# Optimization experiments

Hardware: AMD Instinct MI355X
Metric: run time of the kernel (lower is better)

The kernel has to match this reference:

```python
import jax, jax.numpy as jnp
import numpy as np

MAX_BOXES = 20
IOU_THRESHOLD = 0.1
SCORE_THRESHOLD = 0.3
NUM_CLASSES = 80
N_BOXES = 10647  # YOLOv3 @416: 3*(13^2 + 26^2 + 52^2)


def setup_inputs() -> dict:
    key = jax.random.key(0)
    k1, k2, k3 = jax.random.split(key, 3)
    # boxes in [y1, x1, y2, x2] format (what tf.image.non_max_suppression expects)
    mins = jax.random.uniform(k1, (N_BOXES, 2), minval=0.0, maxval=400.0)
    sizes = jax.random.uniform(k2, (N_BOXES, 2), minval=10.0, maxval=120.0)
    boxes = jnp.concatenate([mins, mins + sizes], axis=1)  # [N,4]
    box_scores = jax.random.uniform(k3, (N_BOXES, NUM_CLASSES))  # [N,C]
    return {"boxes": boxes, "box_scores": box_scores}


def _iou_one_vs_all(box, boxes):
    # box [4], boxes [N,4], format [y1,x1,y2,x2]
    tl = jnp.maximum(box[:2], boxes[:, :2])
    br = jnp.minimum(box[2:], boxes[:, 2:])
    inter = jnp.prod(jnp.clip(br - tl, 0.0), axis=1)
    area1 = jnp.prod(box[2:] - box[:2])
    areas = jnp.prod(boxes[:, 2:] - boxes[:, :2], axis=1)
    union = area1 + areas - inter
    return jnp.where(union > 0, inter / union, 0.0)


def _nms_single_class(boxes, scores):
    """Greedy NMS for one class. Returns padded ([MAX_BOXES] int32 indices, [MAX_BOXES] bool valid).
    Matches tf.image.non_max_suppression semantics (suppress when IoU > threshold),
    applied after the score_threshold mask (invalid scores set to -inf)."""
    n = scores.shape[0]
    s0 = jnp.where(scores >= SCORE_THRESHOLD, scores, -jnp.inf)

    def body(i, state):
        s, idxs, valid = state
        j = jnp.argmax(s)
        ok = s[j] > -jnp.inf
        iou = _iou_one_vs_all(boxes[j], boxes)  # [N]
        suppress = (iou > IOU_THRESHOLD) | (jnp.arange(n) == j)
        s = jnp.where(ok & suppress, -jnp.inf, s)
        idxs = idxs.at[i].set(jnp.where(ok, j, -1).astype(jnp.int32))
        valid = valid.at[i].set(ok)
        return (s, idxs, valid)

    init = (s0, jnp.full((MAX_BOXES,), -1, jnp.int32), jnp.zeros((MAX_BOXES,), bool))
    _, idxs, valid = jax.lax.fori_loop(0, MAX_BOXES, body, init)
    return idxs, valid


def reference(boxes, box_scores):
    # Per-class greedy NMS, vectorized over classes with vmap.
    idxs, valid = jax.vmap(_nms_single_class, in_axes=(None, 1))(boxes, box_scores)  # [C,MAX_BOXES]
    c = box_scores.shape[1]
    classes = jnp.broadcast_to(jnp.arange(c, dtype=jnp.int32)[:, None], (c, MAX_BOXES))
    classes = jnp.where(valid, classes, -1)
    batch_idx = jnp.where(valid, 0, -1).astype(jnp.int32)
    # Fixed-shape (padded) analogue of the variable-length concat in the original:
    # rows are [batch_index, class, box_index]; invalid slots are -1.
    nms_final = jnp.stack([batch_idx, classes, idxs], axis=-1).reshape(1, c * MAX_BOXES, 3)
    boxes_1 = boxes[None]                 # [1,N,4]
    box_scores_t_1 = box_scores.T[None]   # [1,C,N]
    return boxes_1, box_scores_t_1, nms_final
```

## Files before the change

### kernel.cpp

```cpp
#include <hip/hip_runtime.h>
#include <math.h>

#define N_BOXES 10647
#define NUM_CLASSES 80
#define MAX_BOXES 20
#define IOU_T 0.1f
#define SCORE_T 0.3f

#define WND_T 0.992f

#define NT 1024
#define NWAVES (NT / 64)
#define WCAP 128

#define TROWS 64
#define TBLOCKS 167
#define CPBLOCKS 6
#define K1_BLOCKS (TBLOCKS + CPBLOCKS)

#define WSLOTS 8
#define SLOT_N (TBLOCKS * WSLOTS)
#define SENTINEL (~0ull)

#define OUT_OFF_SCORES (N_BOXES * 4)
#define OUT_OFF_NMS (N_BOXES * 4 + NUM_CLASSES * N_BOXES)

#define FOR_K(OP) OP(0) OP(1) OP(2) OP(3) OP(4) OP(5) OP(6) OP(7) OP(8) OP(9) OP(10)

__device__ __forceinline__ bool iou_gt(float jy1, float jx1, float jy2,
                                       float jx2, float area_j, float4 b) {
    float ty = fmaxf(jy1, b.x);
    float tx = fmaxf(jx1, b.y);
    float by = fminf(jy2, b.z);
    float bx = fminf(jx2, b.w);
    float dy = fmaxf(__fsub_rn(by, ty), 0.0f);
    float dx = fmaxf(__fsub_rn(bx, tx), 0.0f);
    float inter = __fmul_rn(dy, dx);
    if (!(inter > 0.0f)) return false;
    float area_i = __fmul_rn(__fsub_rn(b.z, b.x), __fsub_rn(b.w, b.y));
    float uni = __fsub_rn(__fadd_rn(area_j, area_i), inter);
    float iou = (uni > 0.0f) ? __fdiv_rn(inter, uni) : 0.0f;
    return iou > IOU_T;
}

__global__ __launch_bounds__(NT) void transpose_slots_kernel(
    const float* __restrict__ boxes, const float* __restrict__ scores,
    float* __restrict__ out, unsigned long long* __restrict__ ws) {
    const int tid = threadIdx.x;
    const int b = blockIdx.x;

    if (b >= TBLOCKS) {
        for (int q = (b - TBLOCKS) * NT + tid; q < N_BOXES;
             q += CPBLOCKS * NT) {
            ((float4*)out)[q] = ((const float4*)boxes)[q];
        }
        return;
    }

    __shared__ float lds[TROWS * 81];
    const int r0 = b * TROWS;
    const int nr = min(TROWS, N_BOXES - r0);

    const int nq = nr * 20;
    for (int q = tid; q < nq; q += NT) {
        const int r = q / 20;
        const int c4 = (q - r * 20) * 4;
        float4 v = *(const float4*)(scores + (r0 + r) * NUM_CLASSES + c4);
        float* dst = &lds[r * 81 + c4];
        dst[0] = v.x;
        dst[1] = v.y;
        dst[2] = v.z;
        dst[3] = v.w;
    }
    __syncthreads();

    const int r = tid & (TROWS - 1);
    const int chi = tid >> 6;
    #pragma unroll
    for (int p = 0; p < 5; ++p) {
        const int c = p * 16 + chi;
        float v = 0.0f;
        if (r < nr) {
            v = lds[r * 81 + c];
            out[OUT_OFF_SCORES + c * N_BOXES + r0 + r] = v;
        }
        const bool cand = (r < nr) && (v >= WND_T);
        const unsigned long long mask = __ballot(cand);
        unsigned long long* slot = ws + ((size_t)c * TBLOCKS + b) * WSLOTS;
        const int cnt = __popcll(mask);
        if (cnt <= WSLOTS) {
            if (cand) {
                const int rank =
                    __popcll(mask & ((1ull << r) - 1ull));
                slot[rank] =
                    ((unsigned long long)__float_as_uint(v) << 32) |
                    (0xFFFFFFFFu - (unsigned)(r0 + r));
            }
            if (r >= cnt && r < WSLOTS) slot[r] = 0ull;
        } else {
            if (r == 0) slot[0] = SENTINEL;
            if (r >= 1 && r < WSLOTS) slot[r] = 0ull;
        }
    }
}

__global__ __launch_bounds__(NT) void nms_kernel(
    const float* __restrict__ boxes, float* __restrict__ out,
    const unsigned long long* __restrict__ ws) {
    const int tid = threadIdx.x;
    const int c = blockIdx.x;
    const int wave = tid >> 6;
    const int lane = tid & 63;
    const float4* boxes4 = (const float4*)boxes;
    const float* col = out + OUT_OFF_SCORES + c * N_BOXES;

    __shared__ unsigned long long s_k[WCAP];
    __shared__ float4 s_b4[WCAP];
    __shared__ unsigned long long s_ks[WCAP];
    __shared__ float4 s_bs[WCAP];
    __shared__ __align__(16) unsigned long long s_mask[WCAP][2];
    __shared__ unsigned long long s_rk[2][NWAVES];
    __shared__ int s_out[MAX_BOXES];
    __shared__ int s_cnt, s_nsel, s_ovf;

    if (tid < MAX_BOXES) s_out[tid] = -1;
    if (tid == 0) { s_cnt = 0; s_nsel = 0; s_ovf = 0; }
    __syncthreads();

    const unsigned long long* wsl = ws + (size_t)c * SLOT_N;
    for (int q = tid; q < SLOT_N; q += NT) {
        unsigned long long s = wsl[q];
        bool val = false;
        if (s != 0ull) {
            if ((unsigned)(s >> 32) >= 0x3F800000u) {
                s_ovf = 1;
            } else {
                val = true;
            }
        }
        const unsigned long long m = __ballot(val);
        int basew = 0;
        if (lane == 0 && m) basew = atomicAdd(&s_cnt, __popcll(m));
        basew = __shfl(basew, 0);
        if (val) {
            const int pos = basew + __popcll(m & ((1ull << lane) - 1ull));
            if (pos < WCAP) {
                s_k[pos] = s;
                s_b4[pos] = boxes4[0xFFFFFFFFu - (unsigned)s];
            }
        }
    }
    __syncthreads();

    const int wcnt = s_cnt;
    const bool overflow = (wcnt > WCAP) || (s_ovf != 0);

    if (!overflow && tid < wcnt) {
        const unsigned long long mykey = s_k[tid];
        const float4 mybox = s_b4[tid];
        int rank = 0;
        for (int j = 0; j < wcnt; ++j) rank += (s_k[j] > mykey) ? 1 : 0;
        s_ks[rank] = mykey;
        s_bs[rank] = mybox;
    }
    __syncthreads();

    if (!overflow) {
        const int ntask = 2 * wcnt;
        for (int t = wave; t < ntask; t += NWAVES) {
            const int row = t >> 1, ch = t & 1;
            float4 rb = s_bs[row];
            float area_r =
                __fmul_rn(__fsub_rn(rb.z, rb.x), __fsub_rn(rb.w, rb.y));
            int colj = ch * 64 + lane;
            bool s = (colj < wcnt) &&
                     iou_gt(rb.x, rb.y, rb.z, rb.w, area_r, s_bs[colj]);
            unsigned long long m = __ballot(s);
            if (lane == 0) s_mask[row][ch] = m;
        }
    }
    __syncthreads();

    if (wave == 0 && !overflow) {
        unsigned long long a0, a1;
        if (wcnt >= 64) {
            a0 = ~0ull;
            a1 = (wcnt >= 128) ? ~0ull
                               : ((wcnt > 64) ? ((1ull << (wcnt - 64)) - 1)
                                              : 0ull);
        } else {
            a0 = (wcnt > 0) ? ((1ull << wcnt) - 1) : 0ull;
            a1 = 0ull;
        }
        int nkept = 0;
        while ((a0 | a1) != 0 && nkept < MAX_BOXES) {
            int pos = a0 ? __builtin_ctzll(a0)
                         : 64 + __builtin_ctzll(a1);
            if (lane == 0)
                s_out[nkept] =
                    (int)(0xFFFFFFFFu - (unsigned int)s_ks[pos]);
            ++nkept;
            ulonglong2 m = *(const ulonglong2*)&s_mask[pos][0];
            a0 &= ~m.x;
            a1 &= ~m.y;
            if (pos < 64) a0 &= ~(1ull << pos);
            else a1 &= ~(1ull << (pos - 64));
        }
        if (lane == 0) s_nsel = nkept;
    }
    __syncthreads();

    const int nsel0 = s_nsel;
    const bool needs_more = (nsel0 < MAX_BOXES);
    if (needs_more) {
#define DECL_K(k) unsigned long long k_##k = 0;
        FOR_K(DECL_K)
#undef DECL_K
#define BUILDE_K(k)                                                      \
        {                                                                \
            int i = tid + (k)*NT;                                        \
            if (i < N_BOXES) {                                           \
                float v = col[i];                                        \
                if (v >= SCORE_T) {                                      \
                    bool dead = (!overflow && v >= WND_T);               \
                    if (!dead && nsel0 > 0) {                            \
                        float4 bi = boxes4[i];                           \
                        for (int j = 0; j < nsel0; ++j) {                \
                            float4 sb = boxes4[s_out[j]];                \
                            float aj =                                   \
                                __fmul_rn(__fsub_rn(sb.z, sb.x),         \
                                          __fsub_rn(sb.w, sb.y));        \
                            if (iou_gt(sb.x, sb.y, sb.z, sb.w, aj,       \
                                       bi)) {                            \
                                dead = true;                             \
                                break;                                   \
                            }                                            \
                        }                                                \
                    }                                                    \
                    if (!dead)                                           \
                        k_##k = ((unsigned long long)__float_as_uint(v)  \
                                 << 32) |                                \
                                (0xFFFFFFFFu - (unsigned int)i);         \
                }                                                        \
            }                                                            \
        }
        FOR_K(BUILDE_K)
#undef BUILDE_K
        for (int slot = nsel0; slot < MAX_BOXES; ++slot) {
            unsigned long long bk = 0;
#define MAXK_K(k) if (k_##k > bk) bk = k_##k;
            FOR_K(MAXK_K)
#undef MAXK_K
            #pragma unroll
            for (int off = 32; off >= 1; off >>= 1) {
                unsigned long long o =
                    (unsigned long long)__shfl_xor((long long)bk, off);
                if (o > bk) bk = o;
            }
            const int par = slot & 1;
            if (lane == 0) s_rk[par][wave] = bk;
            __syncthreads();
            unsigned long long f = s_rk[par][0];
            #pragma unroll
            for (int w = 1; w < NWAVES; ++w) {
                unsigned long long o = s_rk[par][w];
                if (o > f) f = o;
            }
            if (f == 0) break;
            const int widx = (int)(0xFFFFFFFFu - (unsigned int)f);
            if (tid == 0) s_out[slot] = widx;
            float4 wb = boxes4[widx];
            const float area_j =
                __fmul_rn(__fsub_rn(wb.z, wb.x), __fsub_rn(wb.w, wb.y));
#define SCANE_K(k)                                                      \
            if (k_##k != 0) {                                           \
                int i = tid + (k)*NT;                                   \
                float4 b = boxes4[i];                                   \
                if (i == widx ||                                        \
                    iou_gt(wb.x, wb.y, wb.z, wb.w, area_j, b))          \
                    k_##k = 0;                                          \
            }
            FOR_K(SCANE_K)
#undef SCANE_K
        }
    }

    __syncthreads();
    if (tid < MAX_BOXES) {
        int bi = s_out[tid];
        int o = OUT_OFF_NMS + c * MAX_BOXES * 3 + tid * 3;
        if (bi >= 0) {
            out[o + 0] = 0.0f;
            out[o + 1] = (float)c;
            out[o + 2] = (float)bi;
        } else {
            out[o + 0] = -1.0f;
            out[o + 1] = -1.0f;
            out[o + 2] = -1.0f;
        }
    }
}

extern "C" void kernel_launch(void* const* d_in, const int* in_sizes, int n_in,
                              void* d_out, int out_size, void* d_ws,
                              size_t ws_size, hipStream_t stream) {
    const float* boxes = (const float*)d_in[0];
    const float* scores = (const float*)d_in[1];
    float* out = (float*)d_out;
    unsigned long long* ws = (unsigned long long*)d_ws;

    transpose_slots_kernel<<<K1_BLOCKS, NT, 0, stream>>>(boxes, scores, out,
                                                         ws);
    nms_kernel<<<NUM_CLASSES, NT, 0, stream>>>(boxes, out, ws);
}
```

Before: 71.33 us.

## Fuse transpose and NMS kernels into one launch with global flag handoff

Merges the transpose/candidate-slot kernel and the per-class NMS kernel into a single grid. NMS blocks spin on per-block magic flags published with release stores, so the second launch and its gap go away. Producer blocks also write candidate boxes next to their keys, which removes gathered box loads. The greedy mask walk now keeps masks and keys in registers and reads them with shuffles instead of LDS. This risks deadlock if NMS blocks become resident before producer blocks. Spinning blocks can also occupy CUs, and the flags are never cleared, so a stale-flag problem is possible across calls.

```diff
diff --git a/kernel.cpp b/kernel.cpp
--- a/kernel.cpp
+++ b/kernel.cpp
@@ -15,12 +15,19 @@
 
 #define TROWS 64
 #define TBLOCKS 167
+#define NMSBLOCKS NUM_CLASSES
 #define CPBLOCKS 6
-#define K1_BLOCKS (TBLOCKS + CPBLOCKS)
+#define GRID_BLOCKS (TBLOCKS + NMSBLOCKS + CPBLOCKS)
 
 #define WSLOTS 8
 #define SLOT_N (TBLOCKS * WSLOTS)
+#define KEYS_N (NUM_CLASSES * SLOT_N)
 #define SENTINEL (~0ull)
+
+#define BOX_OFF KEYS_N
+#define FLAG_OFF (KEYS_N * 3)
+#define MAGIC1 0x9E3779B97F4A7C15ull
+#define MAGIC2 0xC2B2AE3D27D4EB4Full
 
 #define OUT_OFF_SCORES (N_BOXES * 4)
 #define OUT_OFF_NMS (N_BOXES * 4 + NUM_CLASSES * N_BOXES)
@@ -43,75 +50,91 @@
     return iou > IOU_T;
 }
 
-__global__ __launch_bounds__(NT) void transpose_slots_kernel(
+__global__ __launch_bounds__(NT) void fused_flag_kernel(
     const float* __restrict__ boxes, const float* __restrict__ scores,
     float* __restrict__ out, unsigned long long* __restrict__ ws) {
     const int tid = threadIdx.x;
     const int b = blockIdx.x;
-
-    if (b >= TBLOCKS) {
-        for (int q = (b - TBLOCKS) * NT + tid; q < N_BOXES;
-             q += CPBLOCKS * NT) {
-            ((float4*)out)[q] = ((const float4*)boxes)[q];
-        }
-        return;
-    }
-
-    __shared__ float lds[TROWS * 81];
-    const int r0 = b * TROWS;
-    const int nr = min(TROWS, N_BOXES - r0);
-
-    const int nq = nr * 20;
-    for (int q = tid; q < nq; q += NT) {
-        const int r = q / 20;
-        const int c4 = (q - r * 20) * 4;
-        float4 v = *(const float4*)(scores + (r0 + r) * NUM_CLASSES + c4);
-        float* dst = &lds[r * 81 + c4];
-        dst[0] = v.x;
-        dst[1] = v.y;
-        dst[2] = v.z;
-        dst[3] = v.w;
-    }
-    __syncthreads();
-
-    const int r = tid & (TROWS - 1);
-    const int chi = tid >> 6;
-    #pragma unroll
-    for (int p = 0; p < 5; ++p) {
-        const int c = p * 16 + chi;
-        float v = 0.0f;
-        if (r < nr) {
-            v = lds[r * 81 + c];
-            out[OUT_OFF_SCORES + c * N_BOXES + r0 + r] = v;
-        }
-        const bool cand = (r < nr) && (v >= WND_T);
-        const unsigned long long mask = __ballot(cand);
-        unsigned long long* slot = ws + ((size_t)c * TBLOCKS + b) * WSLOTS;
-        const int cnt = __popcll(mask);
-        if (cnt <= WSLOTS) {
-            if (cand) {
-                const int rank =
-                    __popcll(mask & ((1ull << r) - 1ull));
-                slot[rank] =
-                    ((unsigned long long)__float_as_uint(v) << 32) |
-                    (0xFFFFFFFFu - (unsigned)(r0 + r));
-            }
-            if (r >= cnt && r < WSLOTS) slot[r] = 0ull;
-        } else {
-            if (r == 0) slot[0] = SENTINEL;
-            if (r >= 1 && r < WSLOTS) slot[r] = 0ull;
-        }
-    }
-}
-
-__global__ __launch_bounds__(NT) void nms_kernel(
-    const float* __restrict__ boxes, float* __restrict__ out,
-    const unsigned long long* __restrict__ ws) {
-    const int tid = threadIdx.x;
-    const int c = blockIdx.x;
     const int wave = tid >> 6;
     const int lane = tid & 63;
     const float4* boxes4 = (const float4*)boxes;
+
+    if (b >= TBLOCKS + NMSBLOCKS) {
+        for (int q = (b - TBLOCKS - NMSBLOCKS) * NT + tid; q < N_BOXES;
+             q += CPBLOCKS * NT) {
+            ((float4*)out)[q] = ((const float4*)boxes)[q];
+        }
+        return;
+    }
+
+    if (b < TBLOCKS) {
+        __shared__ float lds[TROWS * 81];
+        __shared__ float4 s_tb[TROWS];
+        const int r0 = b * TROWS;
+        const int nr = min(TROWS, N_BOXES - r0);
+
+        if (tid < TROWS) {
+            s_tb[tid] = (r0 + tid < N_BOXES) ? boxes4[r0 + tid]
+                                             : make_float4(0.f, 0.f, 0.f, 0.f);
+        }
+
+        const int nq = nr * 20;
+        for (int q = tid; q < nq; q += NT) {
+            const int r = q / 20;
+            const int c4 = (q - r * 20) * 4;
+            float4 v = *(const float4*)(scores + (r0 + r) * NUM_CLASSES + c4);
+            float* dst = &lds[r * 81 + c4];
+            dst[0] = v.x;
+            dst[1] = v.y;
+            dst[2] = v.z;
+            dst[3] = v.w;
+        }
+        __syncthreads();
+
+        unsigned long long* wskeys = ws;
+        float4* wsboxes = (float4*)(ws + BOX_OFF);
+        const int r = tid & (TROWS - 1);
+        const int chi = tid >> 6;
+        #pragma unroll
+        for (int p = 0; p < 5; ++p) {
+            const int c = p * 16 + chi;
+            float v = 0.0f;
+            if (r < nr) {
+                v = lds[r * 81 + c];
+                out[OUT_OFF_SCORES + c * N_BOXES + r0 + r] = v;
+            }
+            const bool cand = (r < nr) && (v >= WND_T);
+            const unsigned long long mask = __ballot(cand);
+            const int cnt = __popcll(mask);
+            const int base = (c * TBLOCKS + b) * WSLOTS;
+            if (cnt <= WSLOTS) {
+                if (cand) {
+                    const int rank = __popcll(mask & ((1ull << r) - 1ull));
+                    wskeys[base + rank] =
+                        ((unsigned long long)__float_as_uint(v) << 32) |
+                        (0xFFFFFFFFu - (unsigned)(r0 + r));
+                    wsboxes[base + rank] = s_tb[r];
+                }
+                if (r >= cnt && r < WSLOTS) wskeys[base + r] = 0ull;
+            } else {
+                if (r == 0) wskeys[base] = SENTINEL;
+                if (r >= 1 && r < WSLOTS) wskeys[base + r] = 0ull;
+            }
+        }
+
+        __syncthreads();
+        if (tid == 0) {
+            __threadfence();
+            unsigned long long* flg = ws + FLAG_OFF;
+            __hip_atomic_store(&flg[2 * b], MAGIC1, __ATOMIC_RELEASE,
+                               __HIP_MEMORY_SCOPE_AGENT);
+            __hip_atomic_store(&flg[2 * b + 1], MAGIC2, __ATOMIC_RELEASE,
+                               __HIP_MEMORY_SCOPE_AGENT);
+        }
+        return;
+    }
+
+    const int c = b - TBLOCKS;
     const float* col = out + OUT_OFF_SCORES + c * N_BOXES;
 
     __shared__ unsigned long long s_k[WCAP];
@@ -125,11 +148,33 @@
 
     if (tid < MAX_BOXES) s_out[tid] = -1;
     if (tid == 0) { s_cnt = 0; s_nsel = 0; s_ovf = 0; }
-    __syncthreads();
-
-    const unsigned long long* wsl = ws + (size_t)c * SLOT_N;
+
+    if (wave == 0) {
+        const unsigned long long* flg = ws + FLAG_OFF;
+        bool ok = false;
+        while (!ok) {
+            bool mine = true;
+            #pragma unroll
+            for (int q = 0; q < 6; ++q) {
+                const int idx = lane + q * 64;
+                if (idx < 2 * TBLOCKS) {
+                    unsigned long long v = __hip_atomic_load(
+                        &flg[idx], __ATOMIC_RELAXED,
+                        __HIP_MEMORY_SCOPE_AGENT);
+                    mine = mine && (v == ((idx & 1) ? MAGIC2 : MAGIC1));
+                }
+            }
+            ok = (__ballot(mine) == ~0ull);
+            if (!ok) __builtin_amdgcn_s_sleep(16);
+        }
+    }
+    __syncthreads();
+    __threadfence();
+
+    const unsigned long long* wsk = ws + (size_t)c * SLOT_N;
+    const float4* wsb = ((const float4*)(ws + BOX_OFF)) + (size_t)c * SLOT_N;
     for (int q = tid; q < SLOT_N; q += NT) {
-        unsigned long long s = wsl[q];
+        unsigned long long s = wsk[q];
         bool val = false;
         if (s != 0ull) {
             if ((unsigned)(s >> 32) >= 0x3F800000u) {
@@ -146,7 +191,7 @@
             const int pos = basew + __popcll(m & ((1ull << lane) - 1ull));
             if (pos < WCAP) {
                 s_k[pos] = s;
-                s_b4[pos] = boxes4[0xFFFFFFFFu - (unsigned)s];
+                s_b4[pos] = wsb[q];
             }
         }
     }
@@ -182,6 +227,12 @@
     __syncthreads();
 
     if (wave == 0 && !overflow) {
+        const unsigned long long pA0 = s_mask[lane][0];
+        const unsigned long long pA1 = s_mask[lane][1];
+        const unsigned long long pB0 = s_mask[64 + lane][0];
+        const unsigned long long pB1 = s_mask[64 + lane][1];
+        const unsigned long long kA = s_ks[lane];
+        const unsigned long long kB = s_ks[64 + lane];
         unsigned long long a0, a1;
         if (wcnt >= 64) {
             a0 = ~0ull;
@@ -194,15 +245,25 @@
         }
         int nkept = 0;
         while ((a0 | a1) != 0 && nkept < MAX_BOXES) {
-            int pos = a0 ? __builtin_ctzll(a0)
-                         : 64 + __builtin_ctzll(a1);
+            int pos;
+            unsigned long long mx, my, kk;
+            if (a0) {
+                pos = __builtin_ctzll(a0);
+                mx = __shfl(pA0, pos);
+                my = __shfl(pA1, pos);
+                kk = __shfl(kA, pos);
+            } else {
+                const int p1 = __builtin_ctzll(a1);
+                mx = __shfl(pB0, p1);
+                my = __shfl(pB1, p1);
+                kk = __shfl(kB, p1);
+                pos = 64 + p1;
+            }
             if (lane == 0)
-                s_out[nkept] =
-                    (int)(0xFFFFFFFFu - (unsigned int)s_ks[pos]);
+                s_out[nkept] = (int)(0xFFFFFFFFu - (unsigned int)kk);
             ++nkept;
-            ulonglong2 m = *(const ulonglong2*)&s_mask[pos][0];
-            a0 &= ~m.x;
-            a1 &= ~m.y;
+            a0 &= ~mx;
+            a1 &= ~my;
             if (pos < 64) a0 &= ~(1ull << pos);
             else a1 &= ~(1ull << (pos - 64));
         }
@@ -246,6 +307,7 @@
         }
         FOR_K(BUILDE_K)
 #undef BUILDE_K
+        #pragma unroll 1
         for (int slot = nsel0; slot < MAX_BOXES; ++slot) {
             unsigned long long bk = 0;
 #define MAXK_K(k) if (k_##k > bk) bk = k_##k;
@@ -275,9 +337,9 @@
 #define SCANE_K(k)                                                      \
             if (k_##k != 0) {                                           \
                 int i = tid + (k)*NT;                                   \
-                float4 b = boxes4[i];                                   \
+                float4 bb = boxes4[i];                                  \
                 if (i == widx ||                                        \
-                    iou_gt(wb.x, wb.y, wb.z, wb.w, area_j, b))          \
+                    iou_gt(wb.x, wb.y, wb.z, wb.w, area_j, bb))         \
                     k_##k = 0;                                          \
             }
             FOR_K(SCANE_K)
@@ -309,7 +371,5 @@
     float* out = (float*)d_out;
     unsigned long long* ws = (unsigned long long*)d_ws;
 
-    transpose_slots_kernel<<<K1_BLOCKS, NT, 0, stream>>>(boxes, scores, out,
-                                                         ws);
-    nms_kernel<<<NUM_CLASSES, NT, 0, stream>>>(boxes, out, ws);
+    fused_flag_kernel<<<GRID_BLOCKS, NT, 0, stream>>>(boxes, scores, out, ws);
 }
```

Result: slower. 99.50 us (+39.5%).
